# Optimization experiments

Measured on AMD Instinct MI355X. Metric: run time of the kernel, lower is better.

## Reference

```python
import jax, jax.numpy as jnp
import numpy as np
from jax import lax

D_VOCAB = 262
D_EMB = 128
CONV_W = 5
PAD = CONV_W // 2  # 2


def setup_inputs() -> dict:
    key = jax.random.key(0)
    k1, k2, k3, k4, k5 = jax.random.split(key, 5)
    B, W, C = 128, 256, 16
    input = jax.random.randint(k1, (B, W, C), 0, D_VOCAB, dtype=jnp.int64)
    lengths = jax.random.randint(k2, (B, W), 1, C + 1, dtype=jnp.int64)
    # torch init: Embedding weight ~ N(0,1) then *0.1
    emb_weight = jax.random.normal(k3, (D_VOCAB, D_EMB), dtype=jnp.float32) * 0.1
    fan_in = D_EMB * CONV_W
    bound = 1.0 / np.sqrt(fan_in)
    conv_w = jax.random.uniform(k4, (D_EMB, D_EMB, CONV_W), dtype=jnp.float32, minval=-bound, maxval=bound)
    conv_b = jax.random.uniform(k5, (D_EMB,), dtype=jnp.float32, minval=-bound, maxval=bound)
    return {"input": input, "lengths": lengths, "emb_weight": emb_weight,
            "conv_w": conv_w, "conv_b": conv_b}


def reference(input, lengths, emb_weight, conv_w, conv_b):
    B, W, C = input.shape
    ids = input.reshape(B * W, C)                      # [N, C]
    embed = emb_weight[ids]                            # [N, C, E] gather
    x = jnp.transpose(embed, (0, 2, 1))                # [N, E, C] (NCW)
    y = lax.conv_general_dilated(
        x, conv_w,
        window_strides=(1,), padding=[(PAD, PAD)],
        dimension_numbers=("NCH", "OIH", "NCH"))       # [N, E, C]
    y = y + conv_b[None, :, None]
    out = jnp.max(y, axis=-1)                          # max-pool over chars
    return out.reshape(B, W, -1)                       # [B, W, E]
```

## Files before the change

kernel.cpp:

```cpp
#include <hip/hip_runtime.h>
#include <hip/hip_fp16.h>

#define D_VOCAB 262
#define D_EMB   128
#define KW      5
#define NCHAR   16
#define NROW    (D_VOCAB * KW)
#define CH      16
#define NCHUNK  (D_EMB / CH)
#define CHUNK_HALFS (NROW * CH)
#define LROW2   10
#define SEQ_PER_BLOCK 256


__global__ __launch_bounds__(256) void transpose_w_kernel(
    const float* __restrict__ cw, float* __restrict__ Wt) {
  const int gid = blockIdx.x * 256 + threadIdx.x;
  const float val = cw[gid];
  const int o = gid / 640;
  const int r = gid - o * 640;
  const int i = r / 5;
  const int k = r - i * 5;
  Wt[(k * D_EMB + o) * D_EMB + i] = val;
}

__global__ __launch_bounds__(256) void compute_P_kernel(
    const float* __restrict__ emb, const float* __restrict__ Wt,
    __half* __restrict__ Pc) {
  const int wave = threadIdx.x >> 6;
  const int lane = threadIdx.x & 63;
  const int w = blockIdx.x * 4 + wave;
  const int v = w / 10;
  const int ko = (w - v * 10) * 64 + lane;

  const float* er = emb + v * D_EMB;
  const float4* wt = (const float4*)(Wt + ko * D_EMB);
  float acc = 0.f;
#pragma unroll 8
  for (int i4 = 0; i4 < 32; ++i4) {
    const float4 wv = wt[i4];
    acc += er[i4 * 4 + 0] * wv.x + er[i4 * 4 + 1] * wv.y +
           er[i4 * 4 + 2] * wv.z + er[i4 * 4 + 3] * wv.w;
  }
  const int k = ko >> 7;
  const int o = ko & 127;
  Pc[(size_t)(o >> 4) * CHUNK_HALFS + (v * KW + k) * CH + (o & 15)] =
      __float2half(acc);
}

__global__ __launch_bounds__(1024, 8) void conv_char_main_kernel(
    const int* __restrict__ ids, const __half* __restrict__ Pc,
    const float* __restrict__ bias, float* __restrict__ out, int n_seq) {
  __shared__ __half2 lds[NROW * LROW2];

  const int t = threadIdx.x;
  const int c = blockIdx.x & (NCHUNK - 1);
  const int seqbase = (blockIdx.x >> 3) * SEQ_PER_BLOCK;

  const int4* src = (const int4*)(Pc + (size_t)c * CHUNK_HALFS);
  for (int t4 = t; t4 < CHUNK_HALFS / 8; t4 += 1024) {
    const int4 v = src[t4];
    const int row = t4 >> 1;
    const int dst = row * LROW2 + (t4 & 1) * 4;
    *(int2*)&lds[dst]     = make_int2(v.x, v.y);
    *(int2*)&lds[dst + 2] = make_int2(v.z, v.w);
  }
  __syncthreads();

  const int wave = t >> 6;
  const int lane = t & 63;
  const int q = lane & 3;
  const int wseq = seqbase + wave * 16;
  const int n = wseq + (lane >> 2);

  int4 myids = make_int4(0, 0, 0, 0);
  if (wseq + (lane >> 2) < n_seq)
    myids = ((const int4*)(ids + (size_t)wseq * NCHAR))[lane];
  const int ida[4] = {myids.x, myids.y, myids.z, myids.w};

  const __half2 hz = __float2half2_rn(0.f);
  __half2 win[5][2];
#pragma unroll
  for (int s = 0; s < 5; ++s) { win[s][0] = hz; win[s][1] = hz; }
  float vmax[4] = {-1e30f, -1e30f, -1e30f, -1e30f};

#pragma unroll
  for (int j = 0; j < NCHAR; ++j) {
    const int idv = __shfl(ida[j & 3], (lane & 60) + (j >> 2));
    const __half2* rp = &lds[idv * (KW * LROW2) + q * 2];
#pragma unroll
    for (int k = 0; k < KW; ++k) {
      const int cc = j + 2 - k;
      if (cc >= 0 && cc < NCHAR) {
        const int2 rv = *(const int2*)(rp + k * LROW2);
        const __half2 a = *(const __half2*)&rv.x;
        const __half2 b = *(const __half2*)&rv.y;
        __half2* ws = win[cc % 5];
        ws[0] = __hadd2(ws[0], a);
        ws[1] = __hadd2(ws[1], b);
      }
    }
    if (j >= 2) {
      const int s = (j - 2) % 5;
      const float2 f0 = __half22float2(win[s][0]);
      const float2 f1 = __half22float2(win[s][1]);
      vmax[0] = fmaxf(vmax[0], f0.x); vmax[1] = fmaxf(vmax[1], f0.y);
      vmax[2] = fmaxf(vmax[2], f1.x); vmax[3] = fmaxf(vmax[3], f1.y);
      win[s][0] = hz; win[s][1] = hz;
    }
  }
#pragma unroll
  for (int cc = 14; cc < 16; ++cc) {
    const int s = cc % 5;
    const float2 f0 = __half22float2(win[s][0]);
    const float2 f1 = __half22float2(win[s][1]);
    vmax[0] = fmaxf(vmax[0], f0.x); vmax[1] = fmaxf(vmax[1], f0.y);
    vmax[2] = fmaxf(vmax[2], f1.x); vmax[3] = fmaxf(vmax[3], f1.y);
  }

  if (n < n_seq) {
    const float4 bv = *(const float4*)(bias + c * CH + q * 4);
    float4 r;
    r.x = vmax[0] + bv.x; r.y = vmax[1] + bv.y;
    r.z = vmax[2] + bv.z; r.w = vmax[3] + bv.w;
    *(float4*)(out + (size_t)n * D_EMB + c * CH + q * 4) = r;
  }
}

extern "C" void kernel_launch(void* const* d_in, const int* in_sizes, int n_in,
                              void* d_out, int out_size, void* d_ws, size_t ws_size,
                              hipStream_t stream) {
  const int*   input = (const int*)d_in[0];
  const float* emb   = (const float*)d_in[2];
  const float* cw    = (const float*)d_in[3];
  const float* cb    = (const float*)d_in[4];
  float* out = (float*)d_out;

  __half* Pc = (__half*)d_ws;
  float*  Wt = (float*)((char*)d_ws + 335872);

  const int n_seq = in_sizes[0] / NCHAR;

  transpose_w_kernel<<<320, 256, 0, stream>>>(cw, Wt);
  compute_P_kernel<<<655, 256, 0, stream>>>(emb, Wt, Pc);

  const int seq_blocks = (n_seq + SEQ_PER_BLOCK - 1) / SEQ_PER_BLOCK;
  conv_char_main_kernel<<<seq_blocks * NCHUNK, 1024, 0, stream>>>(
      input, Pc, cb, out, n_seq);
}
```

Measured before the change: 107.2 us.

## Read precomputed P table directly from global memory instead of LDS chunks

The main kernel no longer stages a 16-channel chunk of the fp16 P table into shared memory per block. Each wave now handles two sequences across all 128 output channels and gathers P rows straight from global memory, relying on L2/L1 caching of the 335 KB table. This removes the per-block LDS fill, the sync and the eightfold redundant id reads across channel chunks, at the cost of scattered global gathers in place of LDS reads. The ids read now assumes an even sequence count, with no bounds check on the load.

```diff
diff --git a/kernel.cpp b/kernel.cpp
--- a/kernel.cpp
+++ b/kernel.cpp
@@ -5,12 +5,7 @@
 #define D_EMB   128
 #define KW      5
 #define NCHAR   16
-#define NROW    (D_VOCAB * KW)
-#define CH      16
-#define NCHUNK  (D_EMB / CH)
-#define CHUNK_HALFS (NROW * CH)
-#define LROW2   10
-#define SEQ_PER_BLOCK 256
+#define NKO     (KW * D_EMB)
 
 
 __global__ __launch_bounds__(256) void transpose_w_kernel(
@@ -26,7 +21,7 @@
 
 __global__ __launch_bounds__(256) void compute_P_kernel(
     const float* __restrict__ emb, const float* __restrict__ Wt,
-    __half* __restrict__ Pc) {
+    __half* __restrict__ P) {
   const int wave = threadIdx.x >> 6;
   const int lane = threadIdx.x & 63;
   const int w = blockIdx.x * 4 + wave;
@@ -42,41 +37,20 @@
     acc += er[i4 * 4 + 0] * wv.x + er[i4 * 4 + 1] * wv.y +
            er[i4 * 4 + 2] * wv.z + er[i4 * 4 + 3] * wv.w;
   }
-  const int k = ko >> 7;
-  const int o = ko & 127;
-  Pc[(size_t)(o >> 4) * CHUNK_HALFS + (v * KW + k) * CH + (o & 15)] =
-      __float2half(acc);
+  P[v * NKO + ko] = __float2half(acc);
 }
 
-__global__ __launch_bounds__(1024, 8) void conv_char_main_kernel(
-    const int* __restrict__ ids, const __half* __restrict__ Pc,
+__global__ __launch_bounds__(256) void conv_char_main_kernel(
+    const int* __restrict__ ids, const __half* __restrict__ P,
     const float* __restrict__ bias, float* __restrict__ out, int n_seq) {
-  __shared__ __half2 lds[NROW * LROW2];
+  const int lane = threadIdx.x & 63;
+  const int w = (blockIdx.x * 256 + threadIdx.x) >> 6;
+  const int n0 = w * 2;
+  const int half = lane >> 5;
+  const int l5 = lane & 31;
+  const int o = l5 * 4;
 
-  const int t = threadIdx.x;
-  const int c = blockIdx.x & (NCHUNK - 1);
-  const int seqbase = (blockIdx.x >> 3) * SEQ_PER_BLOCK;
-
-  const int4* src = (const int4*)(Pc + (size_t)c * CHUNK_HALFS);
-  for (int t4 = t; t4 < CHUNK_HALFS / 8; t4 += 1024) {
-    const int4 v = src[t4];
-    const int row = t4 >> 1;
-    const int dst = row * LROW2 + (t4 & 1) * 4;
-    *(int2*)&lds[dst]     = make_int2(v.x, v.y);
-    *(int2*)&lds[dst + 2] = make_int2(v.z, v.w);
-  }
-  __syncthreads();
-
-  const int wave = t >> 6;
-  const int lane = t & 63;
-  const int q = lane & 3;
-  const int wseq = seqbase + wave * 16;
-  const int n = wseq + (lane >> 2);
-
-  int4 myids = make_int4(0, 0, 0, 0);
-  if (wseq + (lane >> 2) < n_seq)
-    myids = ((const int4*)(ids + (size_t)wseq * NCHAR))[lane];
-  const int ida[4] = {myids.x, myids.y, myids.z, myids.w};
+  const int myid = ids[(size_t)n0 * NCHAR + l5];
 
   const __half2 hz = __float2half2_rn(0.f);
   __half2 win[5][2];
@@ -86,18 +60,16 @@
 
 #pragma unroll
   for (int j = 0; j < NCHAR; ++j) {
-    const int idv = __shfl(ida[j & 3], (lane & 60) + (j >> 2));
-    const __half2* rp = &lds[idv * (KW * LROW2) + q * 2];
+    const int id = __shfl(myid, half * NCHAR + j);
+    const uint2* rp = (const uint2*)(P + (size_t)id * NKO) + l5;
 #pragma unroll
     for (int k = 0; k < KW; ++k) {
       const int cc = j + 2 - k;
       if (cc >= 0 && cc < NCHAR) {
-        const int2 rv = *(const int2*)(rp + k * LROW2);
-        const __half2 a = *(const __half2*)&rv.x;
-        const __half2 b = *(const __half2*)&rv.y;
+        const uint2 rv = rp[k * 32];
         __half2* ws = win[cc % 5];
-        ws[0] = __hadd2(ws[0], a);
-        ws[1] = __hadd2(ws[1], b);
+        ws[0] = __hadd2(ws[0], *(const __half2*)&rv.x);
+        ws[1] = __hadd2(ws[1], *(const __half2*)&rv.y);
       }
     }
     if (j >= 2) {
@@ -118,12 +90,13 @@
     vmax[2] = fmaxf(vmax[2], f1.x); vmax[3] = fmaxf(vmax[3], f1.y);
   }
 
+  const int n = n0 + half;
   if (n < n_seq) {
-    const float4 bv = *(const float4*)(bias + c * CH + q * 4);
+    const float4 bv = *(const float4*)(bias + o);
     float4 r;
     r.x = vmax[0] + bv.x; r.y = vmax[1] + bv.y;
     r.z = vmax[2] + bv.z; r.w = vmax[3] + bv.w;
-    *(float4*)(out + (size_t)n * D_EMB + c * CH + q * 4) = r;
+    *(float4*)(out + (size_t)n * D_EMB + o) = r;
   }
 }
 
@@ -136,15 +109,15 @@
   const float* cb    = (const float*)d_in[4];
   float* out = (float*)d_out;
 
-  __half* Pc = (__half*)d_ws;
+  __half* P  = (__half*)d_ws;
   float*  Wt = (float*)((char*)d_ws + 335872);
 
   const int n_seq = in_sizes[0] / NCHAR;
 
   transpose_w_kernel<<<320, 256, 0, stream>>>(cw, Wt);
-  compute_P_kernel<<<655, 256, 0, stream>>>(emb, Wt, Pc);
+  compute_P_kernel<<<655, 256, 0, stream>>>(emb, Wt, P);
 
-  const int seq_blocks = (n_seq + SEQ_PER_BLOCK - 1) / SEQ_PER_BLOCK;
-  conv_char_main_kernel<<<seq_blocks * NCHUNK, 1024, 0, stream>>>(
-      input, Pc, cb, out, n_seq);
+  const int nwaves = (n_seq + 1) / 2;
+  const int blocks = (nwaves + 3) / 4;
+  conv_char_main_kernel<<<blocks, 256, 0, stream>>>(input, P, cb, out, n_seq);
 }
```

Result: slower. 118.6 us (+10.6%).
